# Kernel tuning notes

Hardware: AMD Instinct MI355X
Metric: run time of the kernel (lower is better)

## Reference

```python
import jax, jax.numpy as jnp
import numpy as np

H = 256                      # neural_renderer default image_size
VIEW_ANGLE = 30.0            # neural_renderer default viewing_angle (deg)
SIGMA = 1e-4                 # soft-rasterizer sharpness for the silhouette
DIST_THRESH = 6.0
NUM_V, NUM_F = 512, 1024


def setup_inputs() -> dict:
    key = jax.random.key(0)
    k1, k2, k3 = jax.random.split(key, 3)
    v = jax.random.uniform(k1, (NUM_V, 3), jnp.float32)
    # normalization from Model.__init__
    v = v - v.min(0)[None, :]
    v = v / jnp.abs(v).max()
    v = v * 2.0
    v = v - v.max(0)[None, :] / 2.0
    vertices = v[None]                                    # [1, V, 3]
    faces = jax.random.randint(k2, (1, NUM_F, 3), 0, NUM_V, jnp.int32)
    image_ref = (jax.random.uniform(k3, (H, H)) > 0.5).astype(jnp.float32)
    camera_position = jnp.array([6.0, 10.0, -14.0], jnp.float32)
    return {"vertices": vertices, "faces": faces,
            "image_ref": image_ref, "camera_position": camera_position}


def _render_silhouette(vertices, faces, eye):
    # --- look_at transform (at=origin, up=+y), as in neural_renderer ---
    def _norm(a):
        return a / (jnp.linalg.norm(a) + 1e-8)
    z_axis = _norm(-eye)
    up = jnp.array([0.0, 1.0, 0.0], eye.dtype)
    x_axis = _norm(jnp.cross(up, z_axis))
    y_axis = _norm(jnp.cross(z_axis, x_axis))
    R = jnp.stack([x_axis, y_axis, z_axis])               # [3, 3]
    v = (vertices - eye) @ R.T                            # [V, 3] camera space
    # --- perspective projection, viewing_angle = 30 deg ---
    t = np.float32(np.tan(np.deg2rad(VIEW_ANGLE)))
    z = v[:, 2]
    xy = v[:, :2] / (z[:, None] * t + 1e-8)               # NDC in [-1, 1]
    tri = xy[faces]                                       # [F, 3, 2]
    tri_z = z[faces]                                      # [F, 3]
    valid = jnp.all(tri_z > 1e-3, axis=1)                 # cull faces behind cam
    # --- pixel grid (row 0 = top, like the rendered image) ---
    c = (jnp.arange(H, dtype=jnp.float32) + 0.5) / H * 2.0 - 1.0
    qx, qy = jnp.meshgrid(c, -c)                          # [H, H]
    q = jnp.stack([qx.ravel(), qy.ravel()], -1)           # [H*W, 2]

    def edge_dist(a, b):
        # signed distance of every pixel to edge a->b, [H*W, F]
        e = b - a                                         # [F, 2]
        inv_len = 1.0 / (jnp.sqrt(jnp.sum(e * e, -1)) + 1e-8)
        cross = (e[None, :, 0] * (q[:, None, 1] - a[None, :, 1])
                 - e[None, :, 1] * (q[:, None, 0] - a[None, :, 0]))
        return cross * inv_len[None, :]

    d0 = edge_dist(tri[:, 0], tri[:, 1])
    d1 = edge_dist(tri[:, 1], tri[:, 2])
    d2 = edge_dist(tri[:, 2], tri[:, 0])
    dmin = jnp.minimum(jnp.minimum(d0, d1), d2)
    dmax = jnp.maximum(jnp.maximum(d0, d1), d2)
    # positive inside the triangle regardless of winding
    dist = jnp.maximum(dmin, -dmax)                       # [H*W, F]
    prob = jax.nn.sigmoid(dist * jnp.abs(dist) / SIGMA)
    prob = jnp.where(valid[None, :], prob, 0.0)
    prob = jnp.clip(prob, 0.0, 1.0 - 1e-6)
    # silhouette alpha = 1 - prod_f (1 - prob_f), computed in log space
    alpha = 1.0 - jnp.exp(jnp.sum(jnp.log1p(-prob), axis=1))
    return alpha.reshape(H, H)[None]                      # [1, H, W]


def reference(vertices, faces, image_ref, camera_position):
    image = _render_silhouette(vertices[0], faces[0], camera_position)
    distance = jnp.linalg.norm(camera_position)
    distance_penalty = jax.nn.relu(DIST_THRESH - distance)
    loss = jnp.sum((image_ref[None] - image) ** 2) * (1.0 + distance_penalty)
    return loss
```

## Files before the change

kernel.cpp:

```cpp
#include <hip/hip_runtime.h>
#include <math.h>

#define NUM_V 512
#define NUM_F 1024
#define IMG_H 256
#define NPIX (IMG_H*IMG_H)
#define NCHUNK 8
#define FPC (NUM_F/NCHUNK)
#define TAN_T 0.57735026919f
#define INV_SIGMA 10000.0f
#define LOG_EPS  -13.8155106f
#define DCULL    -0.0372f

__global__ __launch_bounds__(256, 8) void render_kernel(
    const float* __restrict__ verts,
    const int*   __restrict__ faces,
    const float* __restrict__ cam,
    float* __restrict__ slices,
    float* __restrict__ out)
{
    __shared__ float sx[NUM_V], sy[NUM_V], sz[NUM_V];
    __shared__ float4 sf[(FPC+4)*3];
    __shared__ int scnt;
    const int tid   = threadIdx.x;
    const int chunk = blockIdx.x & (NCHUNK-1);
    const int tile  = blockIdx.x / NCHUNK;

    if (blockIdx.x == 0 && tid == 0) out[0] = 0.0f;
    if (tid == 0) scnt = 0;

    const float ex = cam[0], ey = cam[1], ez = cam[2];
    float inv = 1.0f / (sqrtf(ex*ex + ey*ey + ez*ez) + 1e-8f);
    const float zx = -ex*inv, zy = -ey*inv, zz = -ez*inv;
    float xxr = zz, xyr = 0.0f, xzr = -zx;
    inv = 1.0f / (sqrtf(xxr*xxr + xyr*xyr + xzr*xzr) + 1e-8f);
    const float xx = xxr*inv, xy = xyr*inv, xz = xzr*inv;
    float yxr = zy*xz - zz*xy;
    float yyr = zz*xx - zx*xz;
    float yzr = zx*xy - zy*xx;
    inv = 1.0f / (sqrtf(yxr*yxr + yyr*yyr + yzr*yzr) + 1e-8f);
    const float yx = yxr*inv, yy = yyr*inv, yz = yzr*inv;

    for (int v = tid; v < NUM_V; v += 256) {
        float px = verts[3*v+0] - ex;
        float py = verts[3*v+1] - ey;
        float pz = verts[3*v+2] - ez;
        float vx = xx*px + xy*py + xz*pz;
        float vy = yx*px + yy*py + yz*pz;
        float vz = zx*px + zy*py + zz*pz;
        float denom = 1.0f / (vz*TAN_T + 1e-8f);
        sx[v] = vx*denom;
        sy[v] = vy*denom;
        sz[v] = vz;
    }
    __syncthreads();

    const int j0 = (tile & 15) * 16;
    const int i0 = (tile >> 4) * 16;
    const float xL = (j0 + 0.5f )*(2.0f/IMG_H) - 1.0f;
    const float xR = (j0 + 15.5f)*(2.0f/IMG_H) - 1.0f;
    const float yT = 1.0f - (i0 + 0.5f )*(2.0f/IMG_H);
    const float yB = 1.0f - (i0 + 15.5f)*(2.0f/IMG_H);

    if (tid < FPC) {
        const int f = chunk*FPC + tid;
        int i0f = faces[3*f+0], i1f = faces[3*f+1], i2f = faces[3*f+2];
        float ax = sx[i0f], ay = sy[i0f], z0 = sz[i0f];
        float bx = sx[i1f], by = sy[i1f], z1 = sz[i1f];
        float cx = sx[i2f], cy = sy[i2f], z2 = sz[i2f];
        bool keep = (z0 > 0.001f && z1 > 0.001f && z2 > 0.001f);

        float A[3], B[3], C[3];
        const float px_[3] = {ax, bx, cx}, py_[3] = {ay, by, cy};
        const float qx_[3] = {bx, cx, ax}, qy_[3] = {by, cy, ay};
        #pragma unroll
        for (int k = 0; k < 3; ++k) {
            float eex = qx_[k] - px_[k];
            float eey = qy_[k] - py_[k];
            float il = 1.0f / (sqrtf(eex*eex + eey*eey) + 1e-8f);
            A[k] = eex*il;
            B[k] = eey*il;
            C[k] = (eex*py_[k] - eey*px_[k])*il;
        }

        if (keep) {
            float minmx = 3.0e38f, maxmn = -3.0e38f;
            #pragma unroll
            for (int k = 0; k < 3; ++k) {
                float dTL = A[k]*yT - B[k]*xL - C[k];
                float dTR = A[k]*yT - B[k]*xR - C[k];
                float dBL = A[k]*yB - B[k]*xL - C[k];
                float dBR = A[k]*yB - B[k]*xR - C[k];
                float mx = fmaxf(fmaxf(dTL, dTR), fmaxf(dBL, dBR));
                float mn = fminf(fminf(dTL, dTR), fminf(dBL, dBR));
                minmx = fminf(minmx, mx);
                maxmn = fmaxf(maxmn, mn);
            }
            keep = !((minmx <= DCULL) && (maxmn >= -DCULL));
        }
        if (keep) {
            int s = atomicAdd(&scnt, 1);
            sf[s*3+0] = make_float4(A[0], B[0], C[0], A[1]);
            sf[s*3+1] = make_float4(B[1], C[1], A[2], B[2]);
            sf[s*3+2] = make_float4(C[2], 0.0f, 0.0f, 0.0f);
        }
    }
    __syncthreads();

    int n = scnt;
    const int npad = (4 - (n & 3)) & 3;
    if (tid < npad) {
        const int s = n + tid;
        sf[s*3+0] = make_float4(0.0f, 0.0f, 1e30f, 0.0f);
        sf[s*3+1] = make_float4(0.0f, -1e30f, 0.0f, 0.0f);
        sf[s*3+2] = make_float4(0.0f, 0.0f, 0.0f, 0.0f);
    }
    __syncthreads();
    n = (n + 3) & ~3;

    const int w = tid >> 6, l = tid & 63;
    const int j = j0 + (w & 1)*8 + (l & 7);
    const int i = i0 + (w >> 1)*8 + (l >> 3);
    const int p = i*IMG_H + j;
    const float qx = (j + 0.5f)*(2.0f/IMG_H) - 1.0f;
    const float qy = 1.0f - (i + 0.5f)*(2.0f/IMG_H);

    float acc = 0.0f;
    for (int g = 0; g < n; g += 4) {
        float dist4[4];
        #pragma unroll
        for (int u = 0; u < 4; ++u) {
            float4 w0 = sf[(g+u)*3+0];
            float4 w1 = sf[(g+u)*3+1];
            float4 w2 = sf[(g+u)*3+2];
            float d0 = fmaf(w0.x, qy, -fmaf(w0.y, qx, w0.z));
            float d1 = fmaf(w0.w, qy, -fmaf(w1.x, qx, w1.y));
            float d2 = fmaf(w1.z, qy, -fmaf(w1.w, qx, w2.x));
            float dmin = fminf(fminf(d0, d1), d2);
            float dmax = fmaxf(fmaxf(d0, d1), d2);
            dist4[u] = fmaxf(dmin, -dmax);
        }
        float gm = fmaxf(fmaxf(dist4[0], dist4[1]), fmaxf(dist4[2], dist4[3]));
        if (__any(gm > DCULL)) {
            #pragma unroll
            for (int u = 0; u < 4; ++u) {
                float dist = dist4[u];
                float s  = (dist * INV_SIGMA) * fabsf(dist);
                float e2 = __builtin_exp2f(-fabsf(s) * 1.44269504f);
                float lg = __builtin_log2f(1.0f + e2);
                float sp = fmaf(lg, 0.69314718f, fmaxf(s, 0.0f));
                acc += fmaxf(-sp, LOG_EPS);
            }
        }
    }
    slices[chunk*NPIX + p] = acc;
}

__global__ __launch_bounds__(256) void finalize_kernel(
    const float* __restrict__ image_ref,
    const float* __restrict__ slices,
    const float* __restrict__ cam,
    float* __restrict__ out)
{
    __shared__ float wsum[4];
    const int tid = threadIdx.x;
    const int p = blockIdx.x*256 + tid;

    float lsum = 0.0f;
    #pragma unroll
    for (int c = 0; c < NCHUNK; ++c) lsum += slices[c*NPIX + p];
    float alpha = 1.0f - __expf(lsum);
    float diff  = image_ref[p] - alpha;
    float sq = diff * diff;

    #pragma unroll
    for (int off = 32; off > 0; off >>= 1) sq += __shfl_down(sq, off, 64);
    if ((tid & 63) == 0) wsum[tid >> 6] = sq;
    __syncthreads();
    if (tid == 0) {
        float ex = cam[0], ey = cam[1], ez = cam[2];
        float dist = sqrtf(ex*ex + ey*ey + ez*ez);
        float pen = fmaxf(6.0f - dist, 0.0f);
        float bs = (wsum[0] + wsum[1]) + (wsum[2] + wsum[3]);
        atomicAdd(out, bs * (1.0f + pen));
    }
}

extern "C" void kernel_launch(void* const* d_in, const int* in_sizes, int n_in,
                              void* d_out, int out_size, void* d_ws, size_t ws_size,
                              hipStream_t stream)
{
    const float* verts     = (const float*)d_in[0];
    const int*   faces     = (const int*)  d_in[1];
    const float* image_ref = (const float*)d_in[2];
    const float* cam       = (const float*)d_in[3];

    float* slices = (float*)d_ws;
    float* out    = (float*)d_out;

    render_kernel  <<<256*NCHUNK, 256, 0, stream>>>(verts, faces, cam, slices, out);
    finalize_kernel<<<NPIX/256,   256, 0, stream>>>(image_ref, slices, cam, out);
}
```

Before: 81.10 us.

## Split faces into more chunks, skip empty tile-chunks, fold sigma into edge scale

Doubles the face chunk count so each block handles fewer faces, and records the surviving-face count per tile-chunk so blocks with none exit early without writing slices. The finalize kernel reads those counts and only loads slices for non-empty chunks. Slices move to a tile-contiguous layout. Edge coefficients are prescaled by 100 so the 1/sigma multiply drops out of the inner loop, and the face buffer is split into float4/float4/float arrays to cut shared-memory traffic. More blocks add fixed setup cost per block, since each one recomputes the camera transform and vertex projection.

```diff
diff --git a/kernel.cpp b/kernel.cpp
--- a/kernel.cpp
+++ b/kernel.cpp
@@ -5,22 +5,23 @@
 #define NUM_F 1024
 #define IMG_H 256
 #define NPIX (IMG_H*IMG_H)
-#define NCHUNK 8
+#define NCHUNK 16
 #define FPC (NUM_F/NCHUNK)
 #define TAN_T 0.57735026919f
-#define INV_SIGMA 10000.0f
 #define LOG_EPS  -13.8155106f
-#define DCULL    -0.0372f
+#define DCULL_S  -3.72f
 
 __global__ __launch_bounds__(256, 8) void render_kernel(
     const float* __restrict__ verts,
     const int*   __restrict__ faces,
     const float* __restrict__ cam,
     float* __restrict__ slices,
+    int*   __restrict__ cnt,
     float* __restrict__ out)
 {
     __shared__ float sx[NUM_V], sy[NUM_V], sz[NUM_V];
-    __shared__ float4 sf[(FPC+4)*3];
+    __shared__ float4 sfA[FPC+4], sfB[FPC+4];
+    __shared__ float  sfC[FPC+4];
     __shared__ int scnt;
     const int tid   = threadIdx.x;
     const int chunk = blockIdx.x & (NCHUNK-1);
@@ -77,7 +78,7 @@
         for (int k = 0; k < 3; ++k) {
             float eex = qx_[k] - px_[k];
             float eey = qy_[k] - py_[k];
-            float il = 1.0f / (sqrtf(eex*eex + eey*eey) + 1e-8f);
+            float il = 100.0f / (sqrtf(eex*eex + eey*eey) + 1e-8f);
             A[k] = eex*il;
             B[k] = eey*il;
             C[k] = (eex*py_[k] - eey*px_[k])*il;
@@ -96,56 +97,59 @@
                 minmx = fminf(minmx, mx);
                 maxmn = fmaxf(maxmn, mn);
             }
-            keep = !((minmx <= DCULL) && (maxmn >= -DCULL));
+            keep = !((minmx <= DCULL_S) && (maxmn >= -DCULL_S));
         }
         if (keep) {
             int s = atomicAdd(&scnt, 1);
-            sf[s*3+0] = make_float4(A[0], B[0], C[0], A[1]);
-            sf[s*3+1] = make_float4(B[1], C[1], A[2], B[2]);
-            sf[s*3+2] = make_float4(C[2], 0.0f, 0.0f, 0.0f);
-        }
-    }
-    __syncthreads();
-
-    int n = scnt;
+            sfA[s] = make_float4(A[0], B[0], C[0], A[1]);
+            sfB[s] = make_float4(B[1], C[1], A[2], B[2]);
+            sfC[s] = C[2];
+        }
+    }
+    __syncthreads();
+
+    const int n = scnt;
+    if (tid == 0) cnt[tile*NCHUNK + chunk] = n;
+    if (n == 0) return;
+
     const int npad = (4 - (n & 3)) & 3;
     if (tid < npad) {
         const int s = n + tid;
-        sf[s*3+0] = make_float4(0.0f, 0.0f, 1e30f, 0.0f);
-        sf[s*3+1] = make_float4(0.0f, -1e30f, 0.0f, 0.0f);
-        sf[s*3+2] = make_float4(0.0f, 0.0f, 0.0f, 0.0f);
-    }
-    __syncthreads();
-    n = (n + 3) & ~3;
+        sfA[s] = make_float4(0.0f, 0.0f, 1e30f, 0.0f);
+        sfB[s] = make_float4(0.0f, -1e30f, 0.0f, 0.0f);
+        sfC[s] = 0.0f;
+    }
+    __syncthreads();
+    const int ng = (n + 3) & ~3;
 
     const int w = tid >> 6, l = tid & 63;
-    const int j = j0 + (w & 1)*8 + (l & 7);
-    const int i = i0 + (w >> 1)*8 + (l >> 3);
-    const int p = i*IMG_H + j;
+    const int lj = (w & 1)*8 + (l & 7);
+    const int li = (w >> 1)*8 + (l >> 3);
+    const int j = j0 + lj, i = i0 + li;
     const float qx = (j + 0.5f)*(2.0f/IMG_H) - 1.0f;
     const float qy = 1.0f - (i + 0.5f)*(2.0f/IMG_H);
 
     float acc = 0.0f;
-    for (int g = 0; g < n; g += 4) {
+    for (int g = 0; g < ng; g += 4) {
         float dist4[4];
         #pragma unroll
         for (int u = 0; u < 4; ++u) {
-            float4 w0 = sf[(g+u)*3+0];
-            float4 w1 = sf[(g+u)*3+1];
-            float4 w2 = sf[(g+u)*3+2];
+            float4 w0 = sfA[g+u];
+            float4 w1 = sfB[g+u];
+            float  c2 = sfC[g+u];
             float d0 = fmaf(w0.x, qy, -fmaf(w0.y, qx, w0.z));
             float d1 = fmaf(w0.w, qy, -fmaf(w1.x, qx, w1.y));
-            float d2 = fmaf(w1.z, qy, -fmaf(w1.w, qx, w2.x));
+            float d2 = fmaf(w1.z, qy, -fmaf(w1.w, qx, c2));
             float dmin = fminf(fminf(d0, d1), d2);
             float dmax = fmaxf(fmaxf(d0, d1), d2);
             dist4[u] = fmaxf(dmin, -dmax);
         }
         float gm = fmaxf(fmaxf(dist4[0], dist4[1]), fmaxf(dist4[2], dist4[3]));
-        if (__any(gm > DCULL)) {
+        if (__any(gm > DCULL_S)) {
             #pragma unroll
             for (int u = 0; u < 4; ++u) {
                 float dist = dist4[u];
-                float s  = (dist * INV_SIGMA) * fabsf(dist);
+                float s  = dist * fabsf(dist);
                 float e2 = __builtin_exp2f(-fabsf(s) * 1.44269504f);
                 float lg = __builtin_log2f(1.0f + e2);
                 float sp = fmaf(lg, 0.69314718f, fmaxf(s, 0.0f));
@@ -153,22 +157,30 @@
             }
         }
     }
-    slices[chunk*NPIX + p] = acc;
+    slices[(tile*NCHUNK + chunk)*256 + li*16 + lj] = acc;
 }
 
 __global__ __launch_bounds__(256) void finalize_kernel(
     const float* __restrict__ image_ref,
     const float* __restrict__ slices,
+    const int*   __restrict__ cnt,
     const float* __restrict__ cam,
     float* __restrict__ out)
 {
     __shared__ float wsum[4];
-    const int tid = threadIdx.x;
-    const int p = blockIdx.x*256 + tid;
+    const int tid  = threadIdx.x;
+    const int tile = blockIdx.x;
+    const int j0 = (tile & 15) * 16;
+    const int i0 = (tile >> 4) * 16;
+    const int li = tid >> 4, lj = tid & 15;
+    const int p  = (i0 + li)*IMG_H + (j0 + lj);
 
     float lsum = 0.0f;
     #pragma unroll
-    for (int c = 0; c < NCHUNK; ++c) lsum += slices[c*NPIX + p];
+    for (int c = 0; c < NCHUNK; ++c) {
+        if (cnt[tile*NCHUNK + c] > 0)
+            lsum += slices[(tile*NCHUNK + c)*256 + tid];
+    }
     float alpha = 1.0f - __expf(lsum);
     float diff  = image_ref[p] - alpha;
     float sq = diff * diff;
@@ -196,8 +208,11 @@
     const float* cam       = (const float*)d_in[3];
 
     float* slices = (float*)d_ws;
+    int*   cnt    = (int*)((char*)d_ws + 256*NCHUNK*256*sizeof(float));
     float* out    = (float*)d_out;
 
-    render_kernel  <<<256*NCHUNK, 256, 0, stream>>>(verts, faces, cam, slices, out);
-    finalize_kernel<<<NPIX/256,   256, 0, stream>>>(image_ref, slices, cam, out);
+    render_kernel  <<<256*NCHUNK, 256, 0, stream>>>(verts, faces, cam,
+                                                    slices, cnt, out);
+    finalize_kernel<<<256,        256, 0, stream>>>(image_ref, slices, cnt,
+                                                    cam, out);
 }
```

Measured after the change: 79.51 us (median of 2 runs). -2.0%, faster.
